# Kernel optimization log

Measured on AMD Instinct MI355X. Metric: run time of the kernel, lower is better.

Reference implementation:

```python
import jax, jax.numpy as jnp
import numpy as np

B, C, K, V, S = 16384, 1024, 128, 256, 6
HM, HG, M = 512, 384, 1024
LB = 2
GATE_DIM = C + K + 2 * V + 5  # 1669
CADENCE = 8.0
TEMP = 0.25
REFRESH_T, SPAWN_T, PROMOTE_T, RETIRE_T = 0.55, 0.60, 0.50, 0.15
DECAY = 0.995
EPS_N = 1e-6


def _mlp(x, W1, b1, W2, b2):
    return jax.nn.gelu(x @ W1 + b1, approximate=False) @ W2 + b2


def _l2norm(x):
    n = jnp.linalg.norm(x, axis=-1, keepdims=True)
    return x / jnp.maximum(n, EPS_N)


def setup_inputs():
    key = jax.random.key(0)
    ks = jax.random.split(key, 16)
    p = lambda k, sh: (0.02 * jax.random.normal(k, sh)).astype(jnp.float32)
    return {
        "context": jax.random.normal(ks[0], (B, C), jnp.float32),
        "ledger_bias": jax.random.normal(ks[1], (B, LB), jnp.float32),
        "keys": jax.random.normal(ks[2], (B, S, K), jnp.float32),
        "values": jax.random.normal(ks[3], (B, S, V), jnp.float32),
        "confidence": jax.random.uniform(ks[4], (B, S, 1), jnp.float32),
        "age": 16.0 * jax.random.uniform(ks[5], (B, S, 1), jnp.float32),
        "alive": (jax.random.uniform(ks[6], (B, S, 1)) > 0.3).astype(jnp.float32),
        "Wk1": p(ks[7], (C, HM)), "bk1": jnp.zeros(HM, jnp.float32),
        "Wk2": p(ks[8], (HM, K)), "bk2": jnp.zeros(K, jnp.float32),
        "Wv1": p(ks[9], (C, HM)), "bv1": jnp.zeros(HM, jnp.float32),
        "Wv2": p(ks[10], (HM, V)), "bv2": jnp.zeros(V, jnp.float32),
        "Wg1": p(ks[11], (4, GATE_DIM, HG)), "bg1": jnp.zeros((4, HG), jnp.float32),
        "Wg2": p(ks[12], (4, HG, 1)), "bg2": jnp.zeros((4, 1), jnp.float32),
        "Wsum": p(ks[13], (V, M)), "bsum": jnp.zeros(M, jnp.float32),
        "g_ln": jnp.ones(M, jnp.float32), "b_ln": jnp.zeros(M, jnp.float32),
    }


def _forward(context, ledger_bias, keys, values, confidence, age, alive,
             Wk1, bk1, Wk2, bk2, Wv1, bv1, Wv2, bv2,
             Wg1, bg1, Wg2, bg2, Wsum, bsum, g_ln, b_ln):
    cand_key = _l2norm(_mlp(context, Wk1, bk1, Wk2, bk2))   # [B,K]
    cand_val = _mlp(context, Wv1, bv1, Wv2, bv2)            # [B,V]
    # --- slot match: cosine similarity over live slots, gather best ---
    live = alive[..., 0] > 0                                # [B,S]
    safe_keys = _l2norm(keys + (1.0 - alive) * 1e-4)
    scores = jnp.einsum("bd,bsd->bs", cand_key, safe_keys)
    scores = jnp.where(live, scores, -1e4)
    has_live = jnp.any(live, axis=1, keepdims=True)         # [B,1]
    best_score = jnp.where(has_live, scores.max(axis=1, keepdims=True), 0.0)
    best_index = jnp.where(has_live, jnp.argmax(scores, axis=1, keepdims=True), 0)
    matched_val = jnp.take_along_axis(values, best_index[:, :, None], axis=1)[:, 0]
    matched_age = jnp.take_along_axis(age, best_index[:, :, None], axis=1)[:, 0]
    cadence_prior = jax.nn.sigmoid((matched_age - CADENCE) / CADENCE)
    surprise = 1.0 - best_score
    feats = jnp.concatenate([context, cand_key, cand_val, matched_val,
                             best_score, cadence_prior, surprise, ledger_bias], axis=-1)
    # --- four gate MLPs fused into one batched einsum ---
    h = jax.nn.gelu(jnp.einsum("bf,gfh->bgh", feats, Wg1) + bg1, approximate=False)
    probs = jax.nn.sigmoid(jnp.einsum("bgh,gho->bgo", h, Wg2) + bg2)[:, :, 0]  # [B,4]
    refresh_p, spawn_p, promote_p, retire_p = (probs[:, i:i + 1] for i in range(4))
    # --- soft masks (hard=False path) ---
    has_live_f = alive.max(axis=1)                          # [B,1]
    t = max(TEMP, 1e-4)
    refresh_raw = jax.nn.sigmoid((refresh_p - REFRESH_T) / t) * has_live_f
    spawn_raw = jax.nn.sigmoid((spawn_p - SPAWN_T) / t)
    denom = 1.0 + refresh_raw + spawn_raw
    refresh = refresh_raw / denom
    spawn = spawn_raw / denom
    promote = jax.nn.sigmoid((promote_p - PROMOTE_T) / t)
    retire = jax.nn.sigmoid((retire_p - RETIRE_T) / t)
    # --- spawn slot selection ---
    inactive = (alive[..., 0] < 0.5).astype(jnp.float32)
    has_inactive = inactive.max(axis=1, keepdims=True) > 0.5
    inactive_choice = jnp.argmax(inactive, axis=1, keepdims=True)
    utility = (confidence - 0.01 * age)[..., 0]
    utility = jnp.where(best_index == jnp.arange(S)[None, :], 1e4, utility)
    spawn_index = jnp.where(has_inactive, inactive_choice,
                            jnp.argmin(utility, axis=1, keepdims=True))
    # --- masked scatter update into slot memory ---
    match_hot = jax.nn.one_hot(best_index[:, 0], S, dtype=keys.dtype)[:, :, None]
    spawn_hot = jax.nn.one_hot(spawn_index[:, 0], S, dtype=keys.dtype)[:, :, None]
    refresh_slot = match_hot * refresh[:, None, :]
    spawn_slot = spawn_hot * spawn[:, None, :]
    retire_slot = match_hot * retire[:, None, :]
    write = jnp.clip(refresh_slot + spawn_slot, 0.0, 1.0)
    keys_n = keys * (1.0 - write) + write * cand_key[:, None, :]
    values_n = values * (1.0 - write) + write * cand_val[:, None, :]
    conf_n = (confidence * DECAY * (1.0 - write) + write) * (1.0 - retire_slot)
    age_n = (age + alive) * (1.0 - write)
    alive_n = jnp.clip(alive * (1.0 - retire_slot) + write, 0.0, 1.0)
    # --- confidence-weighted summary + promoted memory token ---
    w = alive_n * conf_n
    summary = (values_n * w).sum(axis=1) / (w.sum(axis=1) + EPS_N)  # [B,V]
    z = summary @ Wsum + bsum
    mu = z.mean(axis=-1, keepdims=True)
    var = ((z - mu) ** 2).mean(axis=-1, keepdims=True)
    promoted = promote * (((z - mu) / jnp.sqrt(var + 1e-5)) * g_ln + b_ln)
    return promoted, summary, keys_n, values_n, conf_n, age_n, alive_n


def reference(context, ledger_bias, keys, values, confidence, age, alive,
              Wk1, bk1, Wk2, bk2, Wv1, bv1, Wv2, bv2,
              Wg1, bg1, Wg2, bg2, Wsum, bsum, g_ln, b_ln):
    return _forward(context, ledger_bias, keys, values, confidence, age, alive,
                    Wk1, bk1, Wk2, bk2, Wv1, bv1, Wv2, bv2,
                    Wg1, bg1, Wg2, bg2, Wsum, bsum, g_ln, b_ln)
```

## Files before the change

### kernel.cpp

```cpp
#include <hip/hip_runtime.h>
#include <math.h>

static constexpr int Bsz  = 16384;
static constexpr int Cdim = 1024;
static constexpr int Kdim = 128;
static constexpr int Vdim = 256;
static constexpr int HMd  = 512;
static constexpr int GOUTd= 1536;
static constexpr int GDIM = 1669;
static constexpr int GPAD = 1728;
static constexpr int F2D  = 704;
static constexpr int Mdim = 1024;
static constexpr float TAU = 2e-3f;

typedef __attribute__((ext_vector_type(8))) _Float16 f16x8;
typedef __attribute__((ext_vector_type(4))) _Float16 f16x4;
typedef __attribute__((ext_vector_type(4))) float f32x4;

__device__ __forceinline__ float sigm(float x){ return 1.0f/(1.0f+__expf(-x)); }
__device__ __forceinline__ float gelu(float x){
    float y = 0.70710678118654752440f * x;
    float a = fabsf(y);
    float t1 = __builtin_amdgcn_rcpf(fmaf(0.3275911f, a, 1.0f));
    float p = t1*fmaf(t1, fmaf(t1, fmaf(t1, fmaf(t1, 1.061405429f, -1.453152027f),
                                         1.421413741f), -0.284496736f), 0.254829592f);
    float e = __expf(-a*a);
    float er = fmaf(-p, e, 1.0f);
    er = (y < 0.0f) ? -er : er;
    return 0.5f*x*(1.0f+er);
}
__device__ __forceinline__ ushort f2h(float f){
    return __builtin_bit_cast(ushort, (_Float16)f);
}
__device__ __forceinline__ unsigned f2q4(float a, float b, float c, float d){
    int v = 0;
    v = __builtin_amdgcn_cvt_pk_fp8_f32(a, b, v, false);
    v = __builtin_amdgcn_cvt_pk_fp8_f32(c, d, v, true);
    return (unsigned)v;
}


__global__ __launch_bounds__(256) void k_zero(int* p){ if (threadIdx.x==0) *p = 0; }

__global__ __launch_bounds__(256) void k_cat(float* __restrict__ dst,
        const float* __restrict__ a, const float* __restrict__ b, int na, int ntot){
    int i = blockIdx.x*256 + threadIdx.x;
    if (i >= ntot) return;
    dst[i] = (i < na) ? a[i] : b[i-na];
}

__global__ __launch_bounds__(256) void k_wt(const float* __restrict__ W,
                                            ushort* __restrict__ Wt, int K, int N){
    __shared__ float tile[64][65];
    int n0 = blockIdx.x*64, k0 = blockIdx.y*64;
    int tx = threadIdx.x & 63, ty = threadIdx.x >> 6;
    #pragma unroll
    for (int i=0;i<64;i+=4)
        tile[ty+i][tx] = W[(size_t)(k0+ty+i)*N + n0 + tx];
    __syncthreads();
    #pragma unroll
    for (int i=0;i<64;i+=4)
        Wt[(size_t)(n0+ty+i)*K + k0 + tx] = f2h(tile[tx][ty+i]);
}

__global__ __launch_bounds__(256) void k_wg1t8(const float* __restrict__ Wg1,
                                               unsigned char* __restrict__ B8){
    int idx = blockIdx.x*256 + threadIdx.x;
    if (idx >= 1536*128) return;
    int n = idx >> 7, ur = idx & 127;
    int g = n / 384, h = n - g*384;
    int f0 = ur*8;
    float v[8];
    #pragma unroll
    for (int j=0;j<8;j++) v[j] = Wg1[((size_t)g*GDIM + f0 + j)*384 + h];
    unsigned q0 = f2q4(v[0],v[1],v[2],v[3]), q1 = f2q4(v[4],v[5],v[6],v[7]);
    int seg = ur >> 4, ul = ur & 15;
    size_t pos = (size_t)n*1024 + seg*128 + (size_t)(ul ^ (n&7))*8;
    ((unsigned*)(B8+pos))[0] = q0;
    ((unsigned*)(B8+pos))[1] = q1;
}

__global__ __launch_bounds__(256) void k_wg1tf(const float* __restrict__ Wg1,
                                               ushort* __restrict__ Wt){
    int idx = blockIdx.x*256 + threadIdx.x;
    if (idx >= 1536*704) return;
    int n = idx / 704, k = idx - n*704;
    int g = n / 384, h = n - g*384;
    int f = 1024 + k;
    float v = (f < GDIM) ? Wg1[((size_t)g*GDIM + f)*384 + h] : 0.0f;
    Wt[(size_t)n*704 + k] = f2h(v);
}

__global__ __launch_bounds__(256) void k_cvt8(const float* __restrict__ x,
        ushort* __restrict__ yh, unsigned char* __restrict__ y8, int nunits){
    int i = blockIdx.x*256 + threadIdx.x;
    if (i >= nunits) return;
    const float4* src = (const float4*)(x + (size_t)i*8);
    float4 v0 = src[0], v1 = src[1];
    ushort4 h0 = { f2h(v0.x), f2h(v0.y), f2h(v0.z), f2h(v0.w) };
    ushort4 h1 = { f2h(v1.x), f2h(v1.y), f2h(v1.z), f2h(v1.w) };
    ((ushort4*)yh)[(size_t)i*2]   = h0;
    ((ushort4*)yh)[(size_t)i*2+1] = h1;
    unsigned q0 = f2q4(v0.x,v0.y,v0.z,v0.w), q1 = f2q4(v1.x,v1.y,v1.z,v1.w);
    int row = i >> 7;
    int ur  = i & 127;
    int seg = ur >> 4, ul = ur & 15;
    size_t pos = (size_t)row*1024 + seg*128 + (size_t)(ul ^ (row&7))*8;
    ((unsigned*)(y8+pos))[0] = q0;
    ((unsigned*)(y8+pos))[1] = q1;
}

__device__ __forceinline__ void gload_lds16(const void* g, void* l){
    typedef __attribute__((address_space(1))) const unsigned gu32;
    typedef __attribute__((address_space(3))) unsigned lu32;
    __builtin_amdgcn_global_load_lds((gu32*)(unsigned long long)g,
                                     (lu32*)(unsigned)(unsigned long long)l,
                                     16, 0, 0);
}

template<int ACT, int OUTM, int SRC, int NX>
__global__ __launch_bounds__(512, 4) void k_mgemm(const ushort* __restrict__ A,
        const ushort* __restrict__ A2, const ushort* __restrict__ Bt,
        const float* __restrict__ bias, const float* __restrict__ Wg2,
        void* __restrict__ Cout, int K, int lda){
    __shared__ alignas(16) ushort lds[24576];
    ushort* As = lds;
    ushort* Bs = lds + 16384;
    int t = threadIdx.x;
    int l = t & 63, wv = t >> 6;
    int wrow = wv >> 1, wcol = wv & 1;
    int nwg = NX * (int)gridDim.y;
    int orig = (int)blockIdx.y * NX + (int)blockIdx.x;
    int qq = nwg >> 3, rr = nwg & 7;
    int xcd = orig & 7, loc = orig >> 3;
    int wgid = (xcd < rr ? xcd*(qq+1) : rr*(qq+1) + (xcd-rr)*qq) + loc;
    int bx = wgid % NX;
    int by = wgid / NX;
    size_t row0 = (size_t)by * 256;
    int col0 = bx * 128;
    constexpr int N = NX*128;
    f32x4 acc[4][4] = {};
    int lrow = l >> 3;
    int lc8  = (l & 7) ^ lrow;

    for (int k0 = 0; k0 < K; k0 += 64){
        const ushort* Ag; size_t astr; int koff;
        if (SRC == 2){
            Ag = A; astr = (size_t)lda; koff = k0 + (bx ? 512 : 0);
        } else { Ag = A; astr = (size_t)lda; koff = k0; }
        #pragma unroll
        for (int i = 0; i < 4; ++i){
            int ch = wv*4 + i;
            int r  = ch*8 + lrow;
            gload_lds16(Ag + (row0 + r)*astr + koff + lc8*8, As + ch*512);
        }
        #pragma unroll
        for (int i = 0; i < 2; ++i){
            int ch = wv*2 + i;
            int r  = ch*8 + lrow;
            gload_lds16(Bt + (size_t)(col0 + r)*K + k0 + lc8*8, Bs + ch*512);
        }
        __syncthreads();
        #pragma unroll
        for (int kk = 0; kk < 2; ++kk){
            f16x8 af[4], bfr[4];
            int j8 = kk*4 + (l >> 4);
            #pragma unroll
            for (int m = 0; m < 4; ++m){
                int row = wrow*64 + m*16 + (l & 15);
                int c16 = j8 ^ (row & 7);
                af[m] = *(const f16x8*)(const void*)(As + row*64 + c16*8);
            }
            #pragma unroll
            for (int n = 0; n < 4; ++n){
                int rowb = wcol*64 + n*16 + (l & 15);
                int c16 = j8 ^ (rowb & 7);
                bfr[n] = *(const f16x8*)(const void*)(Bs + rowb*64 + c16*8);
            }
            #pragma unroll
            for (int m = 0; m < 4; ++m)
                #pragma unroll
                for (int n = 0; n < 4; ++n)
                    acc[m][n] = __builtin_amdgcn_mfma_f32_16x16x32_f16(af[m], bfr[n], acc[m][n], 0, 0, 0);
        }
        __syncthreads();
    }
    int q = l >> 4, cf = l & 15;
    #pragma unroll
    for (int m = 0; m < 4; ++m){
        #pragma unroll
        for (int n = 0; n < 4; ++n){
            int col = col0 + wcol*64 + n*16 + cf;
            float bv = bias[col];
            #pragma unroll
            for (int i = 0; i < 4; ++i){
                size_t r = row0 + wrow*64 + m*16 + q*4 + i;
                float v = acc[m][n][i] + bv;
                if (ACT == 1) v = gelu(v);
                if (OUTM == 1) ((ushort*)Cout)[r*N + col] = f2h(v);
                else           ((float*) Cout)[r*N + col] = v;
            }
        }
    }
}

__global__ __launch_bounds__(512, 4) void k_ggemm(const unsigned char* __restrict__ A8,
        const ushort* __restrict__ Af, const unsigned char* __restrict__ B8,
        const ushort* __restrict__ Bf, const float* __restrict__ bias,
        const float* __restrict__ Wg2, float* __restrict__ part){
    __shared__ alignas(16) unsigned char lds[49152];
    unsigned char* As8 = lds;
    unsigned char* Bs8 = lds + 32768;
    ushort* As16 = (ushort*)lds;
    ushort* Bs16 = (ushort*)(lds + 32768);
    int t = threadIdx.x, l = t & 63, wv = t >> 6;
    int wrow = wv >> 1, wcol = wv & 1;
    constexpr int NX = 12;
    int nwg = NX * (int)gridDim.y;
    int orig = (int)blockIdx.y * NX + (int)blockIdx.x;
    int qq = nwg >> 3, rr = nwg & 7;
    int xcd = orig & 7, loc = orig >> 3;
    int wgid = (xcd < rr ? xcd*(qq+1) : rr*(qq+1) + (xcd-rr)*qq) + loc;
    int bx = wgid % NX;
    int by = wgid / NX;
    size_t row0 = (size_t)by * 256;
    int col0 = bx * 128;
    f32x4 acc[4][4] = {};
    int lrow = l >> 3;

    for (int kt = 0; kt < 8; ++kt){
        int k0 = kt << 7;
        #pragma unroll
        for (int i = 0; i < 4; ++i){
            int ch = wv*4 + i;
            int r  = ch*8 + lrow;
            gload_lds16(A8 + (row0 + r)*1024 + k0 + (l&7)*16, As8 + ch*1024);
        }
        #pragma unroll
        for (int i = 0; i < 2; ++i){
            int ch = wv*2 + i;
            int r  = ch*8 + lrow;
            gload_lds16(B8 + (size_t)(col0 + r)*1024 + k0 + (l&7)*16, Bs8 + ch*1024);
        }
        __syncthreads();
        #pragma unroll
        for (int kk = 0; kk < 4; ++kk){
            long a8[4], b8[4];
            int j8 = (l >> 4) + kk*4;
            #pragma unroll
            for (int m = 0; m < 4; ++m){
                int row = wrow*64 + m*16 + (l & 15);
                int u = j8 ^ (row & 7);
                a8[m] = *(const long*)(const void*)(As8 + row*128 + u*8);
            }
            #pragma unroll
            for (int n = 0; n < 4; ++n){
                int col = wcol*64 + n*16 + (l & 15);
                int u = j8 ^ (col & 7);
                b8[n] = *(const long*)(const void*)(Bs8 + col*128 + u*8);
            }
            #pragma unroll
            for (int m = 0; m < 4; ++m)
                #pragma unroll
                for (int n = 0; n < 4; ++n)
                    acc[m][n] = __builtin_amdgcn_mfma_f32_16x16x32_fp8_fp8(a8[m], b8[n], acc[m][n], 0, 0, 0);
        }
        __syncthreads();
    }
    int lc8 = (l & 7) ^ lrow;
    for (int tt = 0; tt < 11; ++tt){
        int k0 = tt << 6;
        #pragma unroll
        for (int i = 0; i < 4; ++i){
            int ch = wv*4 + i;
            int r  = ch*8 + lrow;
            gload_lds16(Af + (row0 + r)*(size_t)F2D + k0 + lc8*8, As16 + ch*512);
        }
        #pragma unroll
        for (int i = 0; i < 2; ++i){
            int ch = wv*2 + i;
            int r  = ch*8 + lrow;
            gload_lds16(Bf + (size_t)(col0 + r)*F2D + k0 + lc8*8, Bs16 + ch*512);
        }
        __syncthreads();
        #pragma unroll
        for (int kk = 0; kk < 2; ++kk){
            f16x8 af[4], bfr[4];
            int j8 = kk*4 + (l >> 4);
            #pragma unroll
            for (int m = 0; m < 4; ++m){
                int row = wrow*64 + m*16 + (l & 15);
                int c16 = j8 ^ (row & 7);
                af[m] = *(const f16x8*)(const void*)(As16 + row*64 + c16*8);
            }
            #pragma unroll
            for (int n = 0; n < 4; ++n){
                int col = wcol*64 + n*16 + (l & 15);
                int c16 = j8 ^ (col & 7);
                bfr[n] = *(const f16x8*)(const void*)(Bs16 + col*64 + c16*8);
            }
            #pragma unroll
            for (int m = 0; m < 4; ++m)
                #pragma unroll
                for (int n = 0; n < 4; ++n)
                    acc[m][n] = __builtin_amdgcn_mfma_f32_16x16x32_f16(af[m], bfr[n], acc[m][n], 0, 0, 0);
        }
        __syncthreads();
    }
    int q = l >> 4, cf = l & 15;
    float* sacc = (float*)lds;
    if (t < 256) sacc[t] = 0.f;
    __syncthreads();
    #pragma unroll
    for (int m = 0; m < 4; ++m){
        #pragma unroll
        for (int i = 0; i < 4; ++i){
            float v = 0.f;
            #pragma unroll
            for (int n = 0; n < 4; ++n){
                int col = col0 + wcol*64 + n*16 + cf;
                float z = acc[m][n][i] + bias[col];
                v += gelu(z) * Wg2[col];
            }
            atomicAdd(&sacc[wrow*64 + m*16 + q*4 + i], v);
        }
    }
    __syncthreads();
    if (t < 256) part[(row0 + t)*NX + bx] = sacc[t];
}

template<int ACT>
__global__ __launch_bounds__(256) void k_gemm_dyn(const float* __restrict__ A,
                                                  const float* __restrict__ W,
                                                  const float* __restrict__ bias,
                                                  float* __restrict__ C,
                                                  const int* __restrict__ cntp,
                                                  int N, int K){
    int M = (*cntp + 63) & ~63;
    size_t row0 = (size_t)blockIdx.y * 64;
    if ((int)row0 >= M) return;
    __shared__ float As[32][68];
    __shared__ float Ws[32][64];
    int t  = threadIdx.x;
    int tx = t & 15, ty = t >> 4;
    int col0 = blockIdx.x * 64;
    float acc[4][4] = {};
    int ra = t >> 3;
    int ca = (t & 7) << 2;
    int rw = t >> 4;
    int cw = (t & 15) << 2;
    for (int k0 = 0; k0 < K; k0 += 32){
        float4 a0 = *(const float4*)(A + (row0 + ra)*K + k0 + ca);
        float4 a1 = *(const float4*)(A + (row0 + ra + 32)*K + k0 + ca);
        float4 w0 = *(const float4*)(W + (size_t)(k0 + rw)*N + col0 + cw);
        float4 w1 = *(const float4*)(W + (size_t)(k0 + rw + 16)*N + col0 + cw);
        As[ca+0][ra] = a0.x; As[ca+1][ra] = a0.y; As[ca+2][ra] = a0.z; As[ca+3][ra] = a0.w;
        As[ca+0][ra+32] = a1.x; As[ca+1][ra+32] = a1.y; As[ca+2][ra+32] = a1.z; As[ca+3][ra+32] = a1.w;
        *(float4*)&Ws[rw][cw]    = w0;
        *(float4*)&Ws[rw+16][cw] = w1;
        __syncthreads();
        #pragma unroll
        for (int kk = 0; kk < 32; ++kk){
            float4 av = *(const float4*)&As[kk][ty*4];
            float4 wv = *(const float4*)&Ws[kk][tx*4];
            float a4[4] = {av.x, av.y, av.z, av.w};
            float w4[4] = {wv.x, wv.y, wv.z, wv.w};
            #pragma unroll
            for (int i=0;i<4;i++)
                #pragma unroll
                for (int j=0;j<4;j++)
                    acc[i][j] = fmaf(a4[i], w4[j], acc[i][j]);
        }
        __syncthreads();
    }
    #pragma unroll
    for (int i=0;i<4;i++){
        size_t r = row0 + ty*4 + i;
        #pragma unroll
        for (int j=0;j<4;j++){
            int c = col0 + tx*4 + j;
            float v = acc[i][j] + bias[c];
            if (ACT == 1) v = gelu(v);
            C[r*N + c] = v;
        }
    }
}

__global__ __launch_bounds__(256) void k_gather(const float* __restrict__ ctx,
        const int* __restrict__ flaglist, const int* __restrict__ flagcnt,
        float* __restrict__ fctx, int b0){
    int i = (blockIdx.x<<2) + (threadIdx.x>>6);
    int lane = threadIdx.x & 63;
    int cnt = *flagcnt;
    int cntpad = (cnt + 63) & ~63;
    if (i >= cntpad) return;
    float4* dst = (float4*)(fctx + (size_t)i*1024);
    if (i < cnt){
        const float4* src = (const float4*)(ctx + ((size_t)b0 + flaglist[i])*1024);
        #pragma unroll
        for (int j=0;j<4;j++) dst[lane + 64*j] = src[lane + 64*j];
    } else {
        float4 z = {0.f,0.f,0.f,0.f};
        #pragma unroll
        for (int j=0;j<4;j++) dst[lane + 64*j] = z;
    }
}

__global__ __launch_bounds__(256) void k_fixapply(const float* __restrict__ fck,
        const float* __restrict__ keys, const float* __restrict__ values,
        const float* __restrict__ age,  const float* __restrict__ alive,
        float* __restrict__ ckc, ushort* __restrict__ feats2, int* __restrict__ bidx,
        const int* __restrict__ flagcnt, const int* __restrict__ flaglist, int b0){
    int i = (blockIdx.x<<2) + (threadIdx.x>>6);
    int lane = threadIdx.x & 63;
    if (i >= *flagcnt) return;
    int w = flaglist[i];
    size_t b = (size_t)b0 + w;
    float2 c2 = ((const float2*)(fck + (size_t)i*128))[lane];
    float ss = c2.x*c2.x + c2.y*c2.y;
    #pragma unroll
    for (int o=32;o;o>>=1) ss += __shfl_xor(ss,o);
    float inv = 1.0f / fmaxf(sqrtf(ss), 1e-6f);
    float2 cc; cc.x = c2.x*inv; cc.y = c2.y*inv;
    ((float2*)(ckc + (size_t)w*128))[lane] = cc;
    ushort* f2 = feats2 + (size_t)w*F2D;
    { ushort2 o = { f2h(cc.x), f2h(cc.y) };
      ((ushort2*)f2)[lane] = o; }
    float s1v = -1e30f; int bi = 0; int anylive = 0;
    #pragma unroll
    for (int s=0;s<6;s++){
        float a = alive[b*6+s];
        float2 k2 = ((const float2*)(keys + (b*6+s)*128))[lane];
        float ks = k2.x*k2.x + k2.y*k2.y;
        float dt = cc.x*k2.x + cc.y*k2.y;
        #pragma unroll
        for (int o=32;o;o>>=1){ ks += __shfl_xor(ks,o); dt += __shfl_xor(dt,o); }
        float sc;
        if (a > 0.0f){ sc = dt / fmaxf(sqrtf(ks), 1e-6f); anylive = 1; }
        else sc = -1e4f;
        if (sc > s1v){ s1v = sc; bi = s; }
    }
    int bis = anylive ? bi : 0;
    float bsc = anylive ? s1v : 0.0f;
    float4 mv = ((const float4*)(values + (b*6+bis)*256))[lane];
    ushort4 mo = { f2h(mv.x), f2h(mv.y), f2h(mv.z), f2h(mv.w) };
    ((ushort4*)(f2+384))[lane] = mo;
    if (lane == 0){
        bidx[w] = bis;
        float mage = age[b*6 + bis];
        f2[640] = f2h(bsc);
        f2[641] = f2h(sigm((mage - 8.0f)*0.125f));
        f2[642] = f2h(1.0f - bsc);
    }
}

__global__ __launch_bounds__(256) void k_feats(
        const float* __restrict__ ledger, const float* __restrict__ keys,
        const float* __restrict__ values, const float* __restrict__ age,
        const float* __restrict__ alive,  const float* __restrict__ ckv,
        float* __restrict__ ckc, ushort* __restrict__ feats2,
        int* __restrict__ bidx, int* __restrict__ flagcnt, int* __restrict__ flaglist,
        int b0){
    int w = (blockIdx.x<<2) + (threadIdx.x>>6);
    int lane = threadIdx.x & 63;
    size_t b = (size_t)b0 + w;
    const float* ckr = ckv + (size_t)w*384;
    float2 cr2 = ((const float2*)ckr)[lane];
    float ssc = cr2.x*cr2.x + cr2.y*cr2.y;
    #pragma unroll
    for (int o=32;o;o>>=1) ssc += __shfl_xor(ssc,o);
    float invc = 1.0f / fmaxf(sqrtf(ssc), 1e-6f);
    float2 cc; cc.x = cr2.x*invc; cc.y = cr2.y*invc;
    ((float2*)(ckc + (size_t)w*128))[lane] = cc;
    float s1v = -1e30f, s2v = -1e30f; int bi = 0; int anylive = 0;
    #pragma unroll
    for (int s=0;s<6;s++){
        float a = alive[b*6+s];
        float2 k2 = ((const float2*)(keys + (b*6+s)*128))[lane];
        float ss = k2.x*k2.x + k2.y*k2.y;
        float dt = cc.x*k2.x + cc.y*k2.y;
        #pragma unroll
        for (int o=32;o;o>>=1){ ss += __shfl_xor(ss,o); dt += __shfl_xor(dt,o); }
        float sc;
        if (a > 0.0f){ sc = dt / fmaxf(sqrtf(ss), 1e-6f); anylive = 1; }
        else sc = -1e4f;
        if (sc > s1v){ s2v = s1v; s1v = sc; bi = s; }
        else if (sc > s2v) s2v = sc;
    }
    float best_score = anylive ? s1v : 0.0f;
    int bis = anylive ? bi : 0;
    if (lane == 0 && (s1v - s2v) < TAU){
        int pos = atomicAdd(flagcnt, 1);
        flaglist[pos] = w;
    }
    float4 mv = ((const float4*)(values + (b*6+bis)*256))[lane];
    float mage = age[b*6+bis];
    float cad = sigm((mage - 8.0f)*0.125f);
    ushort* f2 = feats2 + (size_t)w*F2D;
    { ushort2 o = { f2h(cc.x), f2h(cc.y) };
      ((ushort2*)f2)[lane] = o; }
    { float4 v = ((const float4*)(ckr+128))[lane];
      ushort4 o = { f2h(v.x), f2h(v.y), f2h(v.z), f2h(v.w) };
      ((ushort4*)(f2+128))[lane] = o; }
    { ushort4 o = { f2h(mv.x), f2h(mv.y), f2h(mv.z), f2h(mv.w) };
      ((ushort4*)(f2+384))[lane] = o; }
    if (lane == 0){
        f2[640] = f2h(best_score);
        f2[641] = f2h(cad);
        f2[642] = f2h(1.0f - best_score);
        f2[643] = f2h(ledger[b*2]);
        f2[644] = f2h(ledger[b*2+1]);
        bidx[w] = bis;
    }
    if (lane < GPAD - GDIM) f2[645+lane] = 0;
}

__global__ __launch_bounds__(256) void k_update(const float* __restrict__ keys,
        const float* __restrict__ values, const float* __restrict__ conf,
        const float* __restrict__ age,    const float* __restrict__ alive,
        const float* __restrict__ ckC,    const float* __restrict__ ckv,
        const float* __restrict__ part,   const float* __restrict__ bg2,
        const int* __restrict__ bidx,
        float* __restrict__ probsC,
        float* __restrict__ o_keys, float* __restrict__ o_vals,
        float* __restrict__ o_conf, float* __restrict__ o_age,
        float* __restrict__ o_aliv, float* __restrict__ o_sum,
        ushort* __restrict__ o_sumb, int b0){
    int w = (blockIdx.x<<2) + (threadIdx.x>>6);
    int lane = threadIdx.x & 63;
    size_t b = (size_t)b0 + w;
    const float* pp = part + (size_t)w*12;
    float pb[4];
    #pragma unroll
    for (int g=0; g<4; ++g)
        pb[g] = sigm(pp[3*g] + pp[3*g+1] + pp[3*g+2] + bg2[g]);
    if (lane < 4) probsC[w*4 + lane] = pb[lane];
    float rp = pb[0], sp = pb[1], tp = pb[3];
    float al[6], cf[6], ag[6];
    float hl = 0.f;
    #pragma unroll
    for (int s=0;s<6;s++){
        al[s]=alive[b*6+s]; cf[s]=conf[b*6+s]; ag[s]=age[b*6+s];
        hl = fmaxf(hl, al[s]);
    }
    float rr = hl * sigm((rp-0.55f)*4.0f);
    float sr = sigm((sp-0.60f)*4.0f);
    float den = 1.0f + rr + sr;
    float refresh = rr/den, spawn = sr/den;
    float retire = sigm((tp-0.15f)*4.0f);
    int bi = bidx[w];
    int ic = -1;
    #pragma unroll
    for (int s=5;s>=0;s--) if (al[s] < 0.5f) ic = s;
    int si;
    if (ic >= 0) si = ic;
    else {
        float bu = 1e30f; int am = 0;
        #pragma unroll
        for (int s=0;s<6;s++){
            float u = (s == bi) ? 1e4f : (cf[s] - 0.01f*ag[s]);
            if (u < bu){ bu = u; am = s; }
        }
        si = am;
    }
    float2 cc  = ((const float2*)(ckC + (size_t)w*128))[lane];
    float4 cvv = ((const float4*)(ckv + (size_t)w*384 + 128))[lane];
    float s0=0,s1=0,s2=0,s3=0, wsum=0;
    #pragma unroll
    for (int s=0;s<6;s++){
        float wr = refresh*(s==bi ? 1.0f:0.0f) + spawn*(s==si ? 1.0f:0.0f);
        wr = fminf(wr, 1.0f);
        float rs = (s==bi) ? retire : 0.0f;
        float om = 1.0f - wr;
        float2 k2 = ((const float2*)(keys + (b*6+s)*128))[lane];
        float2 kn; kn.x = k2.x*om + wr*cc.x; kn.y = k2.y*om + wr*cc.y;
        ((float2*)(o_keys + (b*6+s)*128))[lane] = kn;
        float4 vv = ((const float4*)(values + (b*6+s)*256))[lane];
        float4 vn;
        vn.x = vv.x*om + wr*cvv.x; vn.y = vv.y*om + wr*cvv.y;
        vn.z = vv.z*om + wr*cvv.z; vn.w = vv.w*om + wr*cvv.w;
        ((float4*)(o_vals + (b*6+s)*256))[lane] = vn;
        float cn  = (cf[s]*0.995f*om + wr) * (1.0f - rs);
        float an  = fminf(fmaxf(al[s]*(1.0f - rs) + wr, 0.0f), 1.0f);
        float agn = (ag[s] + al[s]) * om;
        float wgt = an * cn;
        wsum += wgt;
        s0 += vn.x*wgt; s1 += vn.y*wgt; s2 += vn.z*wgt; s3 += vn.w*wgt;
        if (lane == s){ o_conf[b*6+s] = cn; o_age[b*6+s] = agn; o_aliv[b*6+s] = an; }
    }
    float inv = 1.0f/(wsum + 1e-6f);
    float4 sm; sm.x = s0*inv; sm.y = s1*inv; sm.z = s2*inv; sm.w = s3*inv;
    ((float4*)(o_sum + b*256))[lane] = sm;
    ushort4 sb = { f2h(sm.x), f2h(sm.y), f2h(sm.z), f2h(sm.w) };
    ((ushort4*)(o_sumb + (size_t)w*256))[lane] = sb;
}

__global__ __launch_bounds__(256) void k_ln(const ushort* __restrict__ z,
        const float* __restrict__ probs, const float* __restrict__ g_ln,
        const float* __restrict__ b_ln,  float* __restrict__ o_prom, int b0){
    int w = blockIdx.x; int t = threadIdx.x;
    int lane = t & 63, wid = t >> 6;
    f16x4 hv = ((const f16x4*)(z + (size_t)w*1024))[t];
    float v0 = (float)hv[0], v1 = (float)hv[1], v2 = (float)hv[2], v3 = (float)hv[3];
    float s = v0+v1+v2+v3;
    #pragma unroll
    for (int o=32;o;o>>=1) s += __shfl_xor(s,o);
    __shared__ float red[4];
    if (lane==0) red[wid] = s;
    __syncthreads();
    float mu = (red[0]+red[1]+red[2]+red[3]) * (1.0f/1024.0f);
    float d0=v0-mu, d1=v1-mu, d2=v2-mu, d3=v3-mu;
    float ss = d0*d0+d1*d1+d2*d2+d3*d3;
    #pragma unroll
    for (int o=32;o;o>>=1) ss += __shfl_xor(ss,o);
    __syncthreads();
    if (lane==0) red[wid] = ss;
    __syncthreads();
    float var = (red[0]+red[1]+red[2]+red[3]) * (1.0f/1024.0f);
    float rstd = 1.0f / sqrtf(var + 1e-5f);
    float pm = sigm((probs[w*4+2]-0.50f)*4.0f);
    float4 g  = ((const float4*)g_ln)[t];
    float4 bb = ((const float4*)b_ln)[t];
    float4 o;
    o.x = pm*(d0*rstd*g.x + bb.x);
    o.y = pm*(d1*rstd*g.y + bb.y);
    o.z = pm*(d2*rstd*g.z + bb.z);
    o.w = pm*(d3*rstd*g.w + bb.w);
    ((float4*)(o_prom + ((size_t)b0 + w)*1024))[t] = o;
}

extern "C" void kernel_launch(void* const* d_in, const int* in_sizes, int n_in,
                              void* d_out, int out_size, void* d_ws, size_t ws_size,
                              hipStream_t stream){
    const float* ctx    = (const float*)d_in[0];
    const float* ledger = (const float*)d_in[1];
    const float* keys   = (const float*)d_in[2];
    const float* values = (const float*)d_in[3];
    const float* conf   = (const float*)d_in[4];
    const float* age    = (const float*)d_in[5];
    const float* alive  = (const float*)d_in[6];
    const float* Wk1 = (const float*)d_in[7];  const float* bk1 = (const float*)d_in[8];
    const float* Wk2 = (const float*)d_in[9];  const float* bk2 = (const float*)d_in[10];
    const float* Wv1 = (const float*)d_in[11]; const float* bv1 = (const float*)d_in[12];
    const float* Wv2 = (const float*)d_in[13]; const float* bv2 = (const float*)d_in[14];
    const float* Wg1 = (const float*)d_in[15]; const float* bg1 = (const float*)d_in[16];
    const float* Wg2 = (const float*)d_in[17]; const float* bg2 = (const float*)d_in[18];
    const float* Wsum= (const float*)d_in[19]; const float* bsum= (const float*)d_in[20];
    const float* g_ln= (const float*)d_in[21]; const float* b_ln= (const float*)d_in[22];

    float* out   = (float*)d_out;
    float* o_prom= out;
    float* o_sum = o_prom + (size_t)Bsz*Mdim;
    float* o_keys= o_sum  + (size_t)Bsz*Vdim;
    float* o_vals= o_keys + (size_t)Bsz*6*Kdim;
    float* o_conf= o_vals + (size_t)Bsz*6*Vdim;
    float* o_age = o_conf + (size_t)Bsz*6;
    float* o_aliv= o_age  + (size_t)Bsz*6;

    char* p = (char*)d_ws;
    auto alloc = [&](size_t bytes)->char*{
        char* r = p; p += (bytes + 255) & ~(size_t)255; return r;
    };
    ushort* ctxh  = (ushort*)alloc((size_t)Bsz*Cdim*2);
    unsigned char* ctx8 = (unsigned char*)alloc((size_t)Bsz*Cdim);
    ushort* W1m   = (ushort*)alloc((size_t)1024*Cdim*2);
    ushort* W2m   = (ushort*)alloc((size_t)384*HMd*2);
    unsigned char* Wg1t8 = (unsigned char*)alloc((size_t)GOUTd*1024);
    ushort* Wg1tf = (ushort*)alloc((size_t)GOUTd*F2D*2);
    ushort* Wsumt = (ushort*)alloc((size_t)Mdim*Vdim*2);
    float*  biasm1= (float*) alloc(1024*4);
    float*  biasm2= (float*) alloc(384*4);
    size_t fixed = (size_t)(p - (char*)d_ws);
    size_t per_row = 2048 + 1536 + 512 + 1408 + 48 + 4096 + 512 + 16
                   + 4 + 4 + 2048 + 512 + 128;
    int CB = 16384;
    while (CB > 256 && fixed + (size_t)CB*per_row + 16384 > ws_size) CB >>= 1;
    ushort* H      = (ushort*)alloc((size_t)CB*1024*2);
    float*  ckv    = (float*) alloc((size_t)CB*384*4);
    float*  ckc    = (float*) alloc((size_t)CB*Kdim*4);
    ushort* feats2 = (ushort*)alloc((size_t)CB*F2D*2);
    float*  part   = (float*) alloc((size_t)CB*12*4);
    float*  zbuf   = (float*) alloc((size_t)CB*Mdim*4);
    ushort* sumb   = (ushort*)alloc((size_t)CB*Vdim*2);
    float*  probsC = (float*) alloc((size_t)CB*4*4);
    int*    bidxC  = (int*)   alloc((size_t)CB*4);
    int*    flagl  = (int*)   alloc((size_t)CB*4);
    int*    flagc  = (int*)   alloc(256);
    float*  fH     = (float*) alloc((size_t)CB*HMd*4);
    float*  fck    = (float*) alloc((size_t)CB*Kdim*4);
    float*  fctx   = zbuf;
    ushort* zh     = (ushort*)zbuf;

    dim3 blk(256);
    dim3 blk512(512);
    k_cvt8<<<(int)(((size_t)Bsz*Cdim/8 + 255)/256), blk, 0, stream>>>(
        ctx, ctxh, ctx8, (int)((size_t)Bsz*Cdim/8));
    k_wt<<<dim3(HMd/64,  Cdim/64), blk, 0, stream>>>(Wk1, W1m,             Cdim, HMd);
    k_wt<<<dim3(HMd/64,  Cdim/64), blk, 0, stream>>>(Wv1, W1m + 512*Cdim,  Cdim, HMd);
    k_wt<<<dim3(Kdim/64, HMd/64),  blk, 0, stream>>>(Wk2, W2m,             HMd, Kdim);
    k_wt<<<dim3(Vdim/64, HMd/64),  blk, 0, stream>>>(Wv2, W2m + 128*HMd,   HMd, Vdim);
    k_wt<<<dim3(Mdim/64, Vdim/64), blk, 0, stream>>>(Wsum, Wsumt, Vdim, Mdim);
    k_wg1t8<<<(1536*128 + 255)/256, blk, 0, stream>>>(Wg1, Wg1t8);
    k_wg1tf<<<(1536*704 + 255)/256, blk, 0, stream>>>(Wg1, Wg1tf);
    k_cat<<<(1024+255)/256, blk, 0, stream>>>(biasm1, bk1, bv1, 512, 1024);
    k_cat<<<(384+255)/256,  blk, 0, stream>>>(biasm2, bk2, bv2, 128, 384);

    for (int b0 = 0; b0 < Bsz; b0 += CB){
        k_zero<<<1, blk, 0, stream>>>(flagc);
        k_mgemm<1,1,0,8><<<dim3(8, CB/256), blk512, 0, stream>>>(
            ctxh + (size_t)b0*Cdim, nullptr, W1m, biasm1, nullptr, H, Cdim, Cdim);
        k_mgemm<0,0,2,3><<<dim3(3, CB/256), blk512, 0, stream>>>(
            H, nullptr, W2m, biasm2, nullptr, ckv, HMd, 1024);
        k_feats<<<CB/4, blk, 0, stream>>>(ledger, keys, values, age, alive,
                                          ckv, ckc, feats2, bidxC, flagc, flagl, b0);
        k_gather<<<CB/4, blk, 0, stream>>>(ctx, flagl, flagc, fctx, b0);
        k_gemm_dyn<1><<<dim3(HMd/64,  CB/64), blk, 0, stream>>>(fctx, Wk1, bk1, fH,  flagc, HMd,  Cdim);
        k_gemm_dyn<0><<<dim3(Kdim/64, CB/64), blk, 0, stream>>>(fH,   Wk2, bk2, fck, flagc, Kdim, HMd);
        k_fixapply<<<CB/4, blk, 0, stream>>>(fck, keys, values, age, alive,
                                             ckc, feats2, bidxC, flagc, flagl, b0);
        k_ggemm<<<dim3(12, CB/256), blk512, 0, stream>>>(
            ctx8 + (size_t)b0*Cdim, feats2, Wg1t8, Wg1tf, bg1, Wg2, part);
        k_update<<<CB/4, blk, 0, stream>>>(keys, values, conf, age, alive, ckc, ckv,
                                           part, bg2, bidxC, probsC,
                                           o_keys, o_vals, o_conf, o_age, o_aliv,
                                           o_sum, sumb, b0);
        k_mgemm<0,1,0,8><<<dim3(8, CB/256), blk512, 0, stream>>>(
            sumb, nullptr, Wsumt, bsum, nullptr, zh, Vdim, Vdim);
        k_ln<<<CB, blk, 0, stream>>>(zh, probsC, g_ln, b_ln, o_prom, b0);
    }
}
```

Before: 450.9 us.

## Fuse row gather into fallback GEMM and tile Wg1 weight transposes

Drops the separate gather kernel. The first fallback GEMM now reads context rows indirectly through the flag list, which removes a copy to a staging buffer and one launch. The two Wg1 preprocessing kernels are rewritten to go through shared-memory 64x64 tiles, so global reads are coalesced instead of strided by 384 floats. Padded rows now read row b0 rather than zeros, but those outputs are unused.

```diff
diff --git a/kernel.cpp b/kernel.cpp
--- a/kernel.cpp
+++ b/kernel.cpp
@@ -65,30 +65,48 @@
 
 __global__ __launch_bounds__(256) void k_wg1t8(const float* __restrict__ Wg1,
                                                unsigned char* __restrict__ B8){
-    int idx = blockIdx.x*256 + threadIdx.x;
-    if (idx >= 1536*128) return;
-    int n = idx >> 7, ur = idx & 127;
-    int g = n / 384, h = n - g*384;
-    int f0 = ur*8;
-    float v[8];
-    #pragma unroll
-    for (int j=0;j<8;j++) v[j] = Wg1[((size_t)g*GDIM + f0 + j)*384 + h];
-    unsigned q0 = f2q4(v[0],v[1],v[2],v[3]), q1 = f2q4(v[4],v[5],v[6],v[7]);
-    int seg = ur >> 4, ul = ur & 15;
-    size_t pos = (size_t)n*1024 + seg*128 + (size_t)(ul ^ (n&7))*8;
-    ((unsigned*)(B8+pos))[0] = q0;
-    ((unsigned*)(B8+pos))[1] = q1;
+    __shared__ float tile[64][65];
+    int g  = blockIdx.z;
+    int h0 = blockIdx.x*64;
+    int f0 = blockIdx.y*64;
+    int tx = threadIdx.x & 63, ty = threadIdx.x >> 6;
+    #pragma unroll
+    for (int i=0;i<64;i+=4)
+        tile[ty+i][tx] = Wg1[((size_t)g*GDIM + f0+ty+i)*384 + h0+tx];
+    __syncthreads();
+    int u = threadIdx.x & 7, nl0 = threadIdx.x >> 3;
+    #pragma unroll
+    for (int i=0;i<2;i++){
+        int nl = nl0 + i*32;
+        float v[8];
+        #pragma unroll
+        for (int j=0;j<8;j++) v[j] = tile[u*8+j][nl];
+        unsigned q0 = f2q4(v[0],v[1],v[2],v[3]), q1 = f2q4(v[4],v[5],v[6],v[7]);
+        int n  = g*384 + h0 + nl;
+        int ur = (f0>>3) + u;
+        int seg = ur >> 4, ul = ur & 15;
+        size_t pos = (size_t)n*1024 + seg*128 + (size_t)(ul ^ (n&7))*8;
+        ((unsigned*)(B8+pos))[0] = q0;
+        ((unsigned*)(B8+pos))[1] = q1;
+    }
 }
 
 __global__ __launch_bounds__(256) void k_wg1tf(const float* __restrict__ Wg1,
                                                ushort* __restrict__ Wt){
-    int idx = blockIdx.x*256 + threadIdx.x;
-    if (idx >= 1536*704) return;
-    int n = idx / 704, k = idx - n*704;
-    int g = n / 384, h = n - g*384;
-    int f = 1024 + k;
-    float v = (f < GDIM) ? Wg1[((size_t)g*GDIM + f)*384 + h] : 0.0f;
-    Wt[(size_t)n*704 + k] = f2h(v);
+    __shared__ float tile[64][65];
+    int g  = blockIdx.z;
+    int h0 = blockIdx.x*64;
+    int k0 = blockIdx.y*64;
+    int tx = threadIdx.x & 63, ty = threadIdx.x >> 6;
+    #pragma unroll
+    for (int i=0;i<64;i+=4){
+        int f = 1024 + k0 + ty + i;
+        tile[ty+i][tx] = (f < GDIM) ? Wg1[((size_t)g*GDIM + f)*384 + h0+tx] : 0.0f;
+    }
+    __syncthreads();
+    #pragma unroll
+    for (int i=0;i<64;i+=4)
+        Wt[((size_t)(g*384 + h0+ty+i))*F2D + k0 + tx] = f2h(tile[tx][ty+i]);
 }
 
 __global__ __launch_bounds__(256) void k_cvt8(const float* __restrict__ x,
@@ -329,14 +347,16 @@
     if (t < 256) part[(row0 + t)*NX + bx] = sacc[t];
 }
 
-template<int ACT>
+template<int ACT, int GATHER>
 __global__ __launch_bounds__(256) void k_gemm_dyn(const float* __restrict__ A,
                                                   const float* __restrict__ W,
                                                   const float* __restrict__ bias,
                                                   float* __restrict__ C,
                                                   const int* __restrict__ cntp,
-                                                  int N, int K){
-    int M = (*cntp + 63) & ~63;
+                                                  const int* __restrict__ flaglist,
+                                                  int b0, int N, int K){
+    int cnt = *cntp;
+    int M = (cnt + 63) & ~63;
     size_t row0 = (size_t)blockIdx.y * 64;
     if ((int)row0 >= M) return;
     __shared__ float As[32][68];
@@ -349,9 +369,20 @@
     int ca = (t & 7) << 2;
     int rw = t >> 4;
     int cw = (t & 15) << 2;
+    const float *Arow0, *Arow1;
+    if (GATHER){
+        int r1 = (int)row0 + ra, r2 = r1 + 32;
+        int f1 = (r1 < cnt) ? flaglist[r1] : 0;
+        int f2 = (r2 < cnt) ? flaglist[r2] : 0;
+        Arow0 = A + ((size_t)b0 + f1)*K;
+        Arow1 = A + ((size_t)b0 + f2)*K;
+    } else {
+        Arow0 = A + (row0 + ra)*(size_t)K;
+        Arow1 = A + (row0 + ra + 32)*(size_t)K;
+    }
     for (int k0 = 0; k0 < K; k0 += 32){
-        float4 a0 = *(const float4*)(A + (row0 + ra)*K + k0 + ca);
-        float4 a1 = *(const float4*)(A + (row0 + ra + 32)*K + k0 + ca);
+        float4 a0 = *(const float4*)(Arow0 + k0 + ca);
+        float4 a1 = *(const float4*)(Arow1 + k0 + ca);
         float4 w0 = *(const float4*)(W + (size_t)(k0 + rw)*N + col0 + cw);
         float4 w1 = *(const float4*)(W + (size_t)(k0 + rw + 16)*N + col0 + cw);
         As[ca+0][ra] = a0.x; As[ca+1][ra] = a0.y; As[ca+2][ra] = a0.z; As[ca+3][ra] = a0.w;
@@ -383,26 +414,6 @@
             if (ACT == 1) v = gelu(v);
             C[r*N + c] = v;
         }
-    }
-}
-
-__global__ __launch_bounds__(256) void k_gather(const float* __restrict__ ctx,
-        const int* __restrict__ flaglist, const int* __restrict__ flagcnt,
-        float* __restrict__ fctx, int b0){
-    int i = (blockIdx.x<<2) + (threadIdx.x>>6);
-    int lane = threadIdx.x & 63;
-    int cnt = *flagcnt;
-    int cntpad = (cnt + 63) & ~63;
-    if (i >= cntpad) return;
-    float4* dst = (float4*)(fctx + (size_t)i*1024);
-    if (i < cnt){
-        const float4* src = (const float4*)(ctx + ((size_t)b0 + flaglist[i])*1024);
-        #pragma unroll
-        for (int j=0;j<4;j++) dst[lane + 64*j] = src[lane + 64*j];
-    } else {
-        float4 z = {0.f,0.f,0.f,0.f};
-        #pragma unroll
-        for (int j=0;j<4;j++) dst[lane + 64*j] = z;
     }
 }
 
@@ -688,7 +699,6 @@
     int*    flagc  = (int*)   alloc(256);
     float*  fH     = (float*) alloc((size_t)CB*HMd*4);
     float*  fck    = (float*) alloc((size_t)CB*Kdim*4);
-    float*  fctx   = zbuf;
     ushort* zh     = (ushort*)zbuf;
 
     dim3 blk(256);
@@ -700,8 +710,8 @@
     k_wt<<<dim3(Kdim/64, HMd/64),  blk, 0, stream>>>(Wk2, W2m,             HMd, Kdim);
     k_wt<<<dim3(Vdim/64, HMd/64),  blk, 0, stream>>>(Wv2, W2m + 128*HMd,   HMd, Vdim);
     k_wt<<<dim3(Mdim/64, Vdim/64), blk, 0, stream>>>(Wsum, Wsumt, Vdim, Mdim);
-    k_wg1t8<<<(1536*128 + 255)/256, blk, 0, stream>>>(Wg1, Wg1t8);
-    k_wg1tf<<<(1536*704 + 255)/256, blk, 0, stream>>>(Wg1, Wg1tf);
+    k_wg1t8<<<dim3(6, 16, 4), blk, 0, stream>>>(Wg1, Wg1t8);
+    k_wg1tf<<<dim3(6, 11, 4), blk, 0, stream>>>(Wg1, Wg1tf);
     k_cat<<<(1024+255)/256, blk, 0, stream>>>(biasm1, bk1, bv1, 512, 1024);
     k_cat<<<(384+255)/256,  blk, 0, stream>>>(biasm2, bk2, bv2, 128, 384);
 
@@ -713,9 +723,10 @@
             H, nullptr, W2m, biasm2, nullptr, ckv, HMd, 1024);
         k_feats<<<CB/4, blk, 0, stream>>>(ledger, keys, values, age, alive,
                                           ckv, ckc, feats2, bidxC, flagc, flagl, b0);
-        k_gather<<<CB/4, blk, 0, stream>>>(ctx, flagl, flagc, fctx, b0);
-        k_gemm_dyn<1><<<dim3(HMd/64,  CB/64), blk, 0, stream>>>(fctx, Wk1, bk1, fH,  flagc, HMd,  Cdim);
-        k_gemm_dyn<0><<<dim3(Kdim/64, CB/64), blk, 0, stream>>>(fH,   Wk2, bk2, fck, flagc, Kdim, HMd);
+        k_gemm_dyn<1,1><<<dim3(HMd/64,  CB/64), blk, 0, stream>>>(
+            ctx, Wk1, bk1, fH, flagc, flagl, b0, HMd, Cdim);
+        k_gemm_dyn<0,0><<<dim3(Kdim/64, CB/64), blk, 0, stream>>>(
+            fH, Wk2, bk2, fck, flagc, nullptr, 0, Kdim, HMd);
         k_fixapply<<<CB/4, blk, 0, stream>>>(fck, keys, values, age, alive,
                                              ckc, feats2, bidxC, flagc, flagl, b0);
         k_ggemm<<<dim3(12, CB/256), blk512, 0, stream>>>(
```

After: 444.3 us. About the same (-1.5%).
